# Performance work log

Measured on AMD Instinct MI355X. Metric: run time of the kernel, lower is better.

Reference implementation:

```python
import jax, jax.numpy as jnp
import numpy as np

GRID_SIZE = 100
N_GREEN = 524288
N_RED = 524288
LATENT_DIM = 10
HIDDEN = 128
IN_DIM = LATENT_DIM + 3 + 1  # z + level_data + loop index
TEMPERATURE = 500.0


def setup_inputs() -> dict:
    key = jax.random.key(0)
    ks = jax.random.split(key, 13)
    def lin(k, out_d, in_d):
        kw, kb = jax.random.split(k)
        s = 1.0 / np.sqrt(in_d)
        W = jax.random.uniform(kw, (out_d, in_d), jnp.float32, -s, s)
        b = jax.random.uniform(kb, (out_d,), jnp.float32, -s, s)
        return W, b
    z = jax.random.normal(ks[0], (LATENT_DIM,), jnp.float32)
    level_data = jnp.array([GRID_SIZE, N_GREEN, N_RED], dtype=jnp.int64)
    gW1, gb1 = lin(ks[1], HIDDEN, IN_DIM)
    gW2, gb2 = lin(ks[2], HIDDEN, HIDDEN)
    gW3, gb3 = lin(ks[3], 1, HIDDEN)
    rW1, rb1 = lin(ks[4], HIDDEN, IN_DIM)
    rW2, rb2 = lin(ks[5], HIDDEN, HIDDEN)
    rW3, rb3 = lin(ks[6], 1, HIDDEN)
    return {
        'z': z, 'level_data': level_data,
        'gW1': gW1, 'gb1': gb1, 'gW2': gW2, 'gb2': gb2, 'gW3': gW3, 'gb3': gb3,
        'rW1': rW1, 'rb1': rb1, 'rW2': rW2, 'rb2': rb2, 'rW3': rW3, 'rb3': rb3,
    }


def _mlp(x, W1, b1, W2, b2, W3, b3):
    # Linear -> LeakyReLU(0.2) -> Linear -> ELU(alpha=1) -> Linear
    h = jax.nn.leaky_relu(x @ W1.T + b1, negative_slope=0.2)
    h = jax.nn.elu(h @ W2.T + b2, alpha=1.0)
    return h @ W3.T + b3  # [N, 1]


def _coords(z_ext, n, W1, b1, W2, b2, W3, b3, scale):
    # batch all loop indices 0..n-1 into one GEMM call instead of n tiny launches
    idx = jnp.arange(n, dtype=jnp.float32)[:, None]            # [n, 1]
    x = jnp.concatenate(
        [jnp.broadcast_to(z_ext, (n, z_ext.shape[0])), idx], axis=1)  # [n, 14]
    out = _mlp(x, W1, b1, W2, b2, W3, b3)[:, 0]                 # [n]
    return (jax.nn.sigmoid(out / TEMPERATURE) * scale).astype(jnp.int32)


def reference(z, level_data, gW1, gb1, gW2, gb2, gW3, gb3,
              rW1, rb1, rW2, rb2, rW3, rb3):
    scale = level_data[0].astype(jnp.float32) ** 2 - 1.0  # grid_size^2 - 1
    z_ext = jnp.concatenate([z, level_data.astype(jnp.float32)])  # [13]
    coords_green = _coords(z_ext, N_GREEN, gW1, gb1, gW2, gb2, gW3, gb3, scale)
    coords_red = _coords(z_ext, N_RED, rW1, rb1, rW2, rb2, rW3, rb3, scale)
    return coords_green, coords_red
```

## Files before the change

kernel.cpp:

```cpp
#include <hip/hip_runtime.h>
#include <hip/hip_bf16.h>
#include <math.h>


#define HIDDEN 128
#define REGIONS 129
#define NEVT 512
#define CDSTRIDE (NEVT + 8)
#define CHUNK_SH 7
#define WS_HDR 16
#define TIMES_OFF   (WS_HDR)
#define TIMES(g,r)  (TIMES_OFF + ((g)*REGIONS + (r))*NEVT)
#define CTAB_OFF    (TIMES_OFF + 2*REGIONS*NEVT)
#define CTAB(g,r)   (CTAB_OFF + ((g)*REGIONS + (r))*CDSTRIDE)
#define DTAB_OFF    (CTAB_OFF + 2*REGIONS*CDSTRIDE)
#define DTAB(g,r)   (DTAB_OFF + ((g)*REGIONS + (r))*CDSTRIDE)
#define RTS_OFF     (DTAB_OFF + 2*REGIONS*CDSTRIDE)
#define RTS(g)      (RTS_OFF + (g)*REGIONS)
#define DIR_OFF     (RTS_OFF + 2*REGIONS + 16)

__device__ __constant__ float TH[4] = {-4.f, -1.8f, -0.7f, 0.f};
__device__ __constant__ float PM[5] = {0.f, 0.0668106f, 0.3011695f, 0.7191639f, 1.f};
__device__ __constant__ float PQ[5] = {-1.f, -0.7144420f, -0.2925961f, 0.f, 0.f};

__global__ __launch_bounds__(512) void build_kernel(
    const float* __restrict__ z, const int* __restrict__ level,
    const float* __restrict__ gW1, const float* __restrict__ gb1,
    const float* __restrict__ gW2, const float* __restrict__ gb2,
    const float* __restrict__ gW3, const float* __restrict__ gb3,
    const float* __restrict__ rW1, const float* __restrict__ rb1,
    const float* __restrict__ rW2, const float* __restrict__ rb2,
    const float* __restrict__ rW3, const float* __restrict__ rb3,
    float* __restrict__ ws, int* __restrict__ dir, int N, int nchunk)
{
    int g = blockIdx.x / REGIONS;
    int r = blockIdx.x - g * REGIONS;
    const float* W1 = g ? rW1 : gW1;  const float* b1 = g ? rb1 : gb1;
    const float* W2 = g ? rW2 : gW2;  const float* b2 = g ? rb2 : gb2;
    const float* W3 = g ? rW3 : gW3;  const float* b3 = g ? rb3 : gb3;

    __shared__ float zext[16];
    __shared__ float cs[HIDDEN], wv[HIDDEN], tb_l[HIDDEN], sts[HIDDEN];
    __shared__ float sc[HIDDEN], sw[HIDDEN], al[HIDDEN], be[HIDDEN];
    __shared__ float pa[4][HIDDEN], pb[4][HIDDEN];
    __shared__ float ev_t[NEVT], ev_c[NEVT], ev_d[NEVT];
    __shared__ float so_t[NEVT], pc_[NEVT], pd_[NEVT];
    __shared__ float c0s, d0s;
    __shared__ int cnt;
    int t = threadIdx.x;

    if (t == 0) {
        int g0 = level[0], l1 = level[1], l2 = level[2];
        if (l1 == 0) { l1 = level[2]; l2 = level[4]; }
        zext[10] = (float)g0; zext[11] = (float)l1; zext[12] = (float)l2;
        cnt = 0;
        if (blockIdx.x == 0) ws[0] = (float)g0 * (float)g0 - 1.0f;
    }
    if (t < 10) zext[t] = z[t];
    __syncthreads();

    if (t < HIDDEN) {
        float c = b1[t];
        #pragma unroll
        for (int q = 0; q < 13; ++q) c = fmaf(W1[t * 14 + q], zext[q], c);
        float w = W1[t * 14 + 13];
        cs[t] = c; wv[t] = w;
        float Nf = (float)N, tb = -c / w;
        if (!(tb > 0.0f)) tb = 0.0f;
        if (!(tb < Nf))  tb = Nf;
        tb_l[t] = tb;
    }
    __syncthreads();
    if (t < HIDDEN) {
        float tb = tb_l[t]; int rk = 0;
        for (int k = 0; k < HIDDEN; ++k) {
            float tk = tb_l[k];
            rk += (tk < tb || (tk == tb && k < t)) ? 1 : 0;
        }
        sts[rk] = tb;
    }
    __syncthreads();
    float i0 = (r == 0) ? 0.0f : sts[r - 1];
    float i1 = (r == REGIONS - 1) ? (float)N : sts[r];
    if (t == 0) ws[RTS(g) + r] = i1;

    if (t < HIDDEN) {
        float c = cs[t], w = wv[t];
        float mid = 0.5f * (i0 + i1);
        float s = (fmaf(mid, w, c) > 0.0f) ? 1.0f : 0.2f;
        sc[t] = s * c;  sw[t] = s * w;
    }
    __syncthreads();

    {
        int k = t & 127, q = t >> 7;
        float a = 0.0f, bb = 0.0f;
        const float4* row4 = (const float4*)(W2 + k * HIDDEN + q * 32);
        #pragma unroll
        for (int j4 = 0; j4 < 8; ++j4) {
            float4 w2 = row4[j4]; int j = q * 32 + j4 * 4;
            a = fmaf(w2.x, sc[j+0], a);  bb = fmaf(w2.x, sw[j+0], bb);
            a = fmaf(w2.y, sc[j+1], a);  bb = fmaf(w2.y, sw[j+1], bb);
            a = fmaf(w2.z, sc[j+2], a);  bb = fmaf(w2.z, sw[j+2], bb);
            a = fmaf(w2.w, sc[j+3], a);  bb = fmaf(w2.w, sw[j+3], bb);
        }
        pa[q][k] = a;  pb[q][k] = bb;
    }
    __syncthreads();
    if (t < HIDDEN) {
        al[t] = pa[0][t] + pa[1][t] + pa[2][t] + pa[3][t] + b2[t];
        be[t] = pb[0][t] + pb[1][t] + pb[2][t] + pb[3][t];
    }
    __syncthreads();

    {
        int ku = t >> 2, h = t & 3;
        float a = al[ku], b = be[ku], w3 = W3[ku];
        float p0 = fmaf(i0, b, a);
        int pcq = (p0 >= TH[0]) + (p0 >= TH[1]) + (p0 >= TH[2]) + (p0 >= TH[3]);
        bool up = (b > 0.0f), dn = (b < 0.0f);
        bool dir_ok = up ? (h >= pcq) : (dn && (h < pcq));
        float tc = (TH[h] - a) / b;
        if (dir_ok && (tc <= i1)) {
            float dm, dq;
            if (up) { dm = PM[h+1] - PM[h]; dq = PQ[h+1] - PQ[h]; }
            else    { dm = PM[h] - PM[h+1]; dq = PQ[h] - PQ[h+1]; }
            int pos = atomicAdd(&cnt, 1);
            ev_t[pos] = tc;
            ev_c[pos] = w3 * fmaf(dm, a, dq);
            ev_d[pos] = w3 * dm * b;
        }
    }
    if (t < HIDDEN) {
        float a = al[t], b = be[t], w3 = W3[t];
        float p0 = fmaf(i0, b, a);
        int pp = (p0 >= TH[0]) + (p0 >= TH[1]) + (p0 >= TH[2]) + (p0 >= TH[3]);
        pa[0][t] = w3 * fmaf(PM[pp], a, PQ[pp]);
        pb[0][t] = w3 * PM[pp] * b;
    }
    __syncthreads();
    int m = cnt;

    if (t < 64) {
        float sA = pa[0][t] + pa[0][t + 64];
        float sB = pb[0][t] + pb[0][t + 64];
        #pragma unroll
        for (int off = 32; off >= 1; off >>= 1) {
            sA += __shfl_down(sA, off);
            sB += __shfl_down(sB, off);
        }
        if (t == 0) { c0s = sA + b3[0]; d0s = sB; }
    }
    if (t < m) {
        float myt = ev_t[t]; int rk = 0;
        for (int e = 0; e < m; ++e) {
            float te = ev_t[e];
            rk += (te < myt || (te == myt && e < t)) ? 1 : 0;
        }
        so_t[rk] = myt;  pc_[rk] = ev_c[t];  pd_[rk] = ev_d[t];
    }
    __syncthreads();
    if (t == 0) {
        float vc = 0.0f, vd = 0.0f;
        for (int e = 0; e < m; ++e) { vc += pc_[e]; vd += pd_[e]; pc_[e] = vc; pd_[e] = vd; }
    }
    __syncthreads();

    float C0 = c0s, D0 = d0s;
    float totc = (m > 0) ? pc_[m - 1] : 0.0f;
    float totd = (m > 0) ? pd_[m - 1] : 0.0f;
    float* Tt = ws + TIMES(g, r);
    float* Tc = ws + CTAB(g, r);
    float* Td = ws + DTAB(g, r);
    Tt[t]     = (t < m) ? so_t[t] : INFINITY;
    Tc[t + 1] = C0 + ((t < m) ? pc_[t] : totc);
    Td[t + 1] = D0 + ((t < m) ? pd_[t] : totd);
    if (t == 0) { Tc[0] = C0; Td[0] = D0; }

    int qlo = ((int)i0) >> CHUNK_SH;
    for (int q = qlo + t; ; q += 512) {
        float fc = (float)(q << CHUNK_SH);
        if (!(fc < i1)) break;
        if (fc >= i0 && q < nchunk) {
            int a = 0;
            for (int e = 0; e < m; ++e) a += (so_t[e] <= fc) ? 1 : 0;
            dir[g * nchunk + q] = (r << 16) | a;
        }
    }
}

__global__ __launch_bounds__(256) void gen_kernel(
    const float* __restrict__ ws, const int* __restrict__ dir,
    int* __restrict__ out, int N, int total, int nchunk)
{
    int e0 = (blockIdx.x * 256 + threadIdx.x) * 4;
    if (e0 >= total) return;
    int g = (e0 >= N) ? 1 : 0;
    int i = e0 - g * N;

    int pd = dir[g * nchunk + (i >> CHUNK_SH)];
    int r = pd >> 16, a = pd & 0xffff;
    const float* Tt = ws + TIMES(g, r);
    const float* Tc = ws + CTAB(g, r);
    const float* Td = ws + DTAB(g, r);
    const float* RT = ws + RTS(g);
    float rtEnd = RT[r];
    float nextT = Tt[a];
    float C = Tc[a], D = Td[a];
    float scale = ws[0];

    int4 res;
    #pragma unroll
    for (int q = 0; q < 4; ++q) {
        float fi = (float)(i + q);
        while (fi >= rtEnd) {
            ++r; a = 0;
            Tt = ws + TIMES(g, r); Tc = ws + CTAB(g, r); Td = ws + DTAB(g, r);
            rtEnd = RT[r]; nextT = Tt[0]; C = Tc[0]; D = Td[0];
        }
        while (nextT <= fi) {
            ++a; nextT = Tt[a]; C = Tc[a]; D = Td[a];
        }
        float o = fmaf(fi, D, C);
        float sg = 1.0f / (1.0f + __expf(-o * (1.0f / 500.0f)));
        ((int*)&res)[q] = (int)(sg * scale);
    }
    ((int4*)out)[e0 >> 2] = res;
}

extern "C" void kernel_launch(void* const* d_in, const int* in_sizes, int n_in,
                              void* d_out, int out_size, void* d_ws, size_t ws_size,
                              hipStream_t stream) {
    const float* z   = (const float*)d_in[0];
    const int* level = (const int*)d_in[1];
    const float* gW1 = (const float*)d_in[2];
    const float* gb1 = (const float*)d_in[3];
    const float* gW2 = (const float*)d_in[4];
    const float* gb2 = (const float*)d_in[5];
    const float* gW3 = (const float*)d_in[6];
    const float* gb3 = (const float*)d_in[7];
    const float* rW1 = (const float*)d_in[8];
    const float* rb1 = (const float*)d_in[9];
    const float* rW2 = (const float*)d_in[10];
    const float* rb2 = (const float*)d_in[11];
    const float* rW3 = (const float*)d_in[12];
    const float* rb3 = (const float*)d_in[13];
    int* out  = (int*)d_out;
    float* ws = (float*)d_ws;
    int* dir  = (int*)(ws + DIR_OFF);
    int N = out_size / 2;
    int nchunk = (N + (1 << CHUNK_SH) - 1) >> CHUNK_SH;

    build_kernel<<<2 * REGIONS, 512, 0, stream>>>(z, level,
        gW1, gb1, gW2, gb2, gW3, gb3, rW1, rb1, rW2, rb2, rW3, rb3,
        ws, dir, N, nchunk);
    gen_kernel<<<(out_size / 4 + 255) / 256, 256, 0, stream>>>(ws, dir, out,
                                                               N, out_size, nchunk);
}
```

Measured before the change: 94.44 us.

## Fuse build and generate kernels into per-slice piecewise-linear evaluation

Replaces the two-kernel scheme (global region build, then table-driven generation) with one kernel. Each block covers a 1024-element slice and finds the layer-1 breakpoints inside it. For each resulting segment it recomputes the layer-2 affine coefficients and the event list, then evaluates its outputs directly from shared memory. This removes the second launch and the workspace round-trip. In exchange every block of the roughly 1024 launched redoes the W1/W2 matvecs and the event sort per segment, so total compute is much higher.

```diff
diff --git a/kernel.cpp b/kernel.cpp
--- a/kernel.cpp
+++ b/kernel.cpp
@@ -1,29 +1,17 @@
 #include <hip/hip_runtime.h>
-#include <hip/hip_bf16.h>
 #include <math.h>
 
 
 #define HIDDEN 128
-#define REGIONS 129
-#define NEVT 512
-#define CDSTRIDE (NEVT + 8)
-#define CHUNK_SH 7
-#define WS_HDR 16
-#define TIMES_OFF   (WS_HDR)
-#define TIMES(g,r)  (TIMES_OFF + ((g)*REGIONS + (r))*NEVT)
-#define CTAB_OFF    (TIMES_OFF + 2*REGIONS*NEVT)
-#define CTAB(g,r)   (CTAB_OFF + ((g)*REGIONS + (r))*CDSTRIDE)
-#define DTAB_OFF    (CTAB_OFF + 2*REGIONS*CDSTRIDE)
-#define DTAB(g,r)   (DTAB_OFF + ((g)*REGIONS + (r))*CDSTRIDE)
-#define RTS_OFF     (DTAB_OFF + 2*REGIONS*CDSTRIDE)
-#define RTS(g)      (RTS_OFF + (g)*REGIONS)
-#define DIR_OFF     (RTS_OFF + 2*REGIONS + 16)
+#define BLK 256
+#define SLICE 1024
+#define MAXEV 512
 
 __device__ __constant__ float TH[4] = {-4.f, -1.8f, -0.7f, 0.f};
 __device__ __constant__ float PM[5] = {0.f, 0.0668106f, 0.3011695f, 0.7191639f, 1.f};
 __device__ __constant__ float PQ[5] = {-1.f, -0.7144420f, -0.2925961f, 0.f, 0.f};
 
-__global__ __launch_bounds__(512) void build_kernel(
+__global__ __launch_bounds__(BLK) void fused_kernel(
     const float* __restrict__ z, const int* __restrict__ level,
     const float* __restrict__ gW1, const float* __restrict__ gb1,
     const float* __restrict__ gW2, const float* __restrict__ gb2,
@@ -31,30 +19,36 @@
     const float* __restrict__ rW1, const float* __restrict__ rb1,
     const float* __restrict__ rW2, const float* __restrict__ rb2,
     const float* __restrict__ rW3, const float* __restrict__ rb3,
-    float* __restrict__ ws, int* __restrict__ dir, int N, int nchunk)
+    int* __restrict__ out, int N, int total)
 {
-    int g = blockIdx.x / REGIONS;
-    int r = blockIdx.x - g * REGIONS;
+    __shared__ float zext[16];
+    __shared__ float cs[HIDDEN], wv[HIDDEN];
+    __shared__ float sc[HIDDEN], sw[HIDDEN], al[HIDDEN], be[HIDDEN];
+    __shared__ float pA[2][HIDDEN], pB[2][HIDDEN];
+    __shared__ float sA[HIDDEN], sB[HIDDEN];
+    __shared__ float bps[HIDDEN], bss[HIDDEN];
+    __shared__ float ev_t[MAXEV], ev_c[MAXEV], ev_d[MAXEV];
+    __shared__ float so_t[MAXEV], pc_[MAXEV], pd_[MAXEV];
+    __shared__ float c0s, d0s;
+    __shared__ int cnt, bcnt;
+
+    int t = threadIdx.x;
+    int gbase = blockIdx.x * SLICE;
+    int g = (gbase >= N) ? 1 : 0;
+    int s0 = gbase - g * N;
+    int s1 = s0 + SLICE; if (s1 > N) s1 = N;
+    float s0f = (float)s0, s1f = (float)s1;
+
     const float* W1 = g ? rW1 : gW1;  const float* b1 = g ? rb1 : gb1;
     const float* W2 = g ? rW2 : gW2;  const float* b2 = g ? rb2 : gb2;
     const float* W3 = g ? rW3 : gW3;  const float* b3 = g ? rb3 : gb3;
-
-    __shared__ float zext[16];
-    __shared__ float cs[HIDDEN], wv[HIDDEN], tb_l[HIDDEN], sts[HIDDEN];
-    __shared__ float sc[HIDDEN], sw[HIDDEN], al[HIDDEN], be[HIDDEN];
-    __shared__ float pa[4][HIDDEN], pb[4][HIDDEN];
-    __shared__ float ev_t[NEVT], ev_c[NEVT], ev_d[NEVT];
-    __shared__ float so_t[NEVT], pc_[NEVT], pd_[NEVT];
-    __shared__ float c0s, d0s;
-    __shared__ int cnt;
-    int t = threadIdx.x;
 
     if (t == 0) {
         int g0 = level[0], l1 = level[1], l2 = level[2];
         if (l1 == 0) { l1 = level[2]; l2 = level[4]; }
         zext[10] = (float)g0; zext[11] = (float)l1; zext[12] = (float)l2;
-        cnt = 0;
-        if (blockIdx.x == 0) ws[0] = (float)g0 * (float)g0 - 1.0f;
+        zext[13] = (float)g0 * (float)g0 - 1.0f;
+        bcnt = 0;
     }
     if (t < 10) zext[t] = z[t];
     __syncthreads();
@@ -65,167 +59,133 @@
         for (int q = 0; q < 13; ++q) c = fmaf(W1[t * 14 + q], zext[q], c);
         float w = W1[t * 14 + 13];
         cs[t] = c; wv[t] = w;
-        float Nf = (float)N, tb = -c / w;
-        if (!(tb > 0.0f)) tb = 0.0f;
-        if (!(tb < Nf))  tb = Nf;
-        tb_l[t] = tb;
+        float tb = -c / w;
+        if (tb > s0f && tb < s1f) {
+            int p = atomicAdd(&bcnt, 1);
+            bps[p] = tb;
+        }
     }
     __syncthreads();
-    if (t < HIDDEN) {
-        float tb = tb_l[t]; int rk = 0;
-        for (int k = 0; k < HIDDEN; ++k) {
-            float tk = tb_l[k];
-            rk += (tk < tb || (tk == tb && k < t)) ? 1 : 0;
-        }
-        sts[rk] = tb;
+    int nb = bcnt;
+    if (t < nb) {
+        float myt = bps[t]; int rk = 0;
+        for (int e = 0; e < nb; ++e) {
+            float te = bps[e];
+            rk += (te < myt || (te == myt && e < t)) ? 1 : 0;
+        }
+        bss[rk] = myt;
     }
     __syncthreads();
-    float i0 = (r == 0) ? 0.0f : sts[r - 1];
-    float i1 = (r == REGIONS - 1) ? (float)N : sts[r];
-    if (t == 0) ws[RTS(g) + r] = i1;
-
-    if (t < HIDDEN) {
-        float c = cs[t], w = wv[t];
-        float mid = 0.5f * (i0 + i1);
-        float s = (fmaf(mid, w, c) > 0.0f) ? 1.0f : 0.2f;
-        sc[t] = s * c;  sw[t] = s * w;
-    }
-    __syncthreads();
-
-    {
-        int k = t & 127, q = t >> 7;
-        float a = 0.0f, bb = 0.0f;
-        const float4* row4 = (const float4*)(W2 + k * HIDDEN + q * 32);
+
+    float scale = zext[13];
+    int4 res = make_int4(0, 0, 0, 0);
+    int ibase = s0 + t * 4;
+
+    for (int seg = 0; seg <= nb; ++seg) {
+        float i0 = (seg == 0) ? s0f : bss[seg - 1];
+        float i1 = (seg == nb) ? s1f : bss[seg];
+
+        if (t < HIDDEN) {
+            float mid = 0.5f * (i0 + i1);
+            float s = (fmaf(mid, wv[t], cs[t]) > 0.0f) ? 1.0f : 0.2f;
+            sc[t] = s * cs[t];  sw[t] = s * wv[t];
+        }
+        if (t == 0) cnt = 0;
+        __syncthreads();
+
+        {
+            int k = t & 127, qq = t >> 7;
+            float a = 0.0f, bb = 0.0f;
+            const float4* row4 = (const float4*)(W2 + k * HIDDEN + qq * 64);
+            #pragma unroll
+            for (int j4 = 0; j4 < 16; ++j4) {
+                float4 w2 = row4[j4]; int j = qq * 64 + j4 * 4;
+                a = fmaf(w2.x, sc[j+0], a);  bb = fmaf(w2.x, sw[j+0], bb);
+                a = fmaf(w2.y, sc[j+1], a);  bb = fmaf(w2.y, sw[j+1], bb);
+                a = fmaf(w2.z, sc[j+2], a);  bb = fmaf(w2.z, sw[j+2], bb);
+                a = fmaf(w2.w, sc[j+3], a);  bb = fmaf(w2.w, sw[j+3], bb);
+            }
+            pA[qq][k] = a;  pB[qq][k] = bb;
+        }
+        __syncthreads();
+        if (t < HIDDEN) {
+            al[t] = pA[0][t] + pA[1][t] + b2[t];
+            be[t] = pB[0][t] + pB[1][t];
+        }
+        __syncthreads();
+
+        for (int e = t; e < 512; e += BLK) {
+            int ku = e >> 2, h = e & 3;
+            float a = al[ku], b = be[ku], w3 = W3[ku];
+            float p0 = fmaf(i0, b, a);
+            int pcq = (p0 >= TH[0]) + (p0 >= TH[1]) + (p0 >= TH[2]) + (p0 >= TH[3]);
+            bool up = (b > 0.0f), dn = (b < 0.0f);
+            bool ok = up ? (h >= pcq) : (dn && (h < pcq));
+            float tc = (TH[h] - a) / b;
+            if (ok && tc <= i1) {
+                float dm, dq;
+                if (up) { dm = PM[h+1] - PM[h]; dq = PQ[h+1] - PQ[h]; }
+                else    { dm = PM[h] - PM[h+1]; dq = PQ[h] - PQ[h+1]; }
+                int pos = atomicAdd(&cnt, 1);
+                ev_t[pos] = tc;
+                ev_c[pos] = w3 * fmaf(dm, a, dq);
+                ev_d[pos] = w3 * dm * b;
+            }
+        }
+        if (t < HIDDEN) {
+            float a = al[t], b = be[t], w3 = W3[t];
+            float p0 = fmaf(i0, b, a);
+            int pp = (p0 >= TH[0]) + (p0 >= TH[1]) + (p0 >= TH[2]) + (p0 >= TH[3]);
+            sA[t] = w3 * fmaf(PM[pp], a, PQ[pp]);
+            sB[t] = w3 * PM[pp] * b;
+        }
+        __syncthreads();
+        int m = cnt;
+
+        if (t < 64) {
+            float rA = sA[t] + sA[t + 64];
+            float rB = sB[t] + sB[t + 64];
+            #pragma unroll
+            for (int off = 32; off >= 1; off >>= 1) {
+                rA += __shfl_down(rA, off);
+                rB += __shfl_down(rB, off);
+            }
+            if (t == 0) { c0s = rA + b3[0]; d0s = rB; }
+        }
+        for (int ei = t; ei < m; ei += BLK) {
+            float myt = ev_t[ei]; int rk = 0;
+            for (int e = 0; e < m; ++e) {
+                float te = ev_t[e];
+                rk += (te < myt || (te == myt && e < ei)) ? 1 : 0;
+            }
+            so_t[rk] = myt;  pc_[rk] = ev_c[ei];  pd_[rk] = ev_d[ei];
+        }
+        __syncthreads();
+        if (t == 0) {
+            float vc = 0.0f, vd = 0.0f;
+            for (int e = 0; e < m; ++e) { vc += pc_[e]; vd += pd_[e]; pc_[e] = vc; pd_[e] = vd; }
+        }
+        __syncthreads();
+
+        float C0 = c0s, D0 = d0s;
         #pragma unroll
-        for (int j4 = 0; j4 < 8; ++j4) {
-            float4 w2 = row4[j4]; int j = q * 32 + j4 * 4;
-            a = fmaf(w2.x, sc[j+0], a);  bb = fmaf(w2.x, sw[j+0], bb);
-            a = fmaf(w2.y, sc[j+1], a);  bb = fmaf(w2.y, sw[j+1], bb);
-            a = fmaf(w2.z, sc[j+2], a);  bb = fmaf(w2.z, sw[j+2], bb);
-            a = fmaf(w2.w, sc[j+3], a);  bb = fmaf(w2.w, sw[j+3], bb);
-        }
-        pa[q][k] = a;  pb[q][k] = bb;
-    }
-    __syncthreads();
-    if (t < HIDDEN) {
-        al[t] = pa[0][t] + pa[1][t] + pa[2][t] + pa[3][t] + b2[t];
-        be[t] = pb[0][t] + pb[1][t] + pb[2][t] + pb[3][t];
-    }
-    __syncthreads();
-
-    {
-        int ku = t >> 2, h = t & 3;
-        float a = al[ku], b = be[ku], w3 = W3[ku];
-        float p0 = fmaf(i0, b, a);
-        int pcq = (p0 >= TH[0]) + (p0 >= TH[1]) + (p0 >= TH[2]) + (p0 >= TH[3]);
-        bool up = (b > 0.0f), dn = (b < 0.0f);
-        bool dir_ok = up ? (h >= pcq) : (dn && (h < pcq));
-        float tc = (TH[h] - a) / b;
-        if (dir_ok && (tc <= i1)) {
-            float dm, dq;
-            if (up) { dm = PM[h+1] - PM[h]; dq = PQ[h+1] - PQ[h]; }
-            else    { dm = PM[h] - PM[h+1]; dq = PQ[h] - PQ[h+1]; }
-            int pos = atomicAdd(&cnt, 1);
-            ev_t[pos] = tc;
-            ev_c[pos] = w3 * fmaf(dm, a, dq);
-            ev_d[pos] = w3 * dm * b;
-        }
-    }
-    if (t < HIDDEN) {
-        float a = al[t], b = be[t], w3 = W3[t];
-        float p0 = fmaf(i0, b, a);
-        int pp = (p0 >= TH[0]) + (p0 >= TH[1]) + (p0 >= TH[2]) + (p0 >= TH[3]);
-        pa[0][t] = w3 * fmaf(PM[pp], a, PQ[pp]);
-        pb[0][t] = w3 * PM[pp] * b;
-    }
-    __syncthreads();
-    int m = cnt;
-
-    if (t < 64) {
-        float sA = pa[0][t] + pa[0][t + 64];
-        float sB = pb[0][t] + pb[0][t + 64];
-        #pragma unroll
-        for (int off = 32; off >= 1; off >>= 1) {
-            sA += __shfl_down(sA, off);
-            sB += __shfl_down(sB, off);
-        }
-        if (t == 0) { c0s = sA + b3[0]; d0s = sB; }
-    }
-    if (t < m) {
-        float myt = ev_t[t]; int rk = 0;
-        for (int e = 0; e < m; ++e) {
-            float te = ev_t[e];
-            rk += (te < myt || (te == myt && e < t)) ? 1 : 0;
-        }
-        so_t[rk] = myt;  pc_[rk] = ev_c[t];  pd_[rk] = ev_d[t];
-    }
-    __syncthreads();
-    if (t == 0) {
-        float vc = 0.0f, vd = 0.0f;
-        for (int e = 0; e < m; ++e) { vc += pc_[e]; vd += pd_[e]; pc_[e] = vc; pd_[e] = vd; }
-    }
-    __syncthreads();
-
-    float C0 = c0s, D0 = d0s;
-    float totc = (m > 0) ? pc_[m - 1] : 0.0f;
-    float totd = (m > 0) ? pd_[m - 1] : 0.0f;
-    float* Tt = ws + TIMES(g, r);
-    float* Tc = ws + CTAB(g, r);
-    float* Td = ws + DTAB(g, r);
-    Tt[t]     = (t < m) ? so_t[t] : INFINITY;
-    Tc[t + 1] = C0 + ((t < m) ? pc_[t] : totc);
-    Td[t + 1] = D0 + ((t < m) ? pd_[t] : totd);
-    if (t == 0) { Tc[0] = C0; Td[0] = D0; }
-
-    int qlo = ((int)i0) >> CHUNK_SH;
-    for (int q = qlo + t; ; q += 512) {
-        float fc = (float)(q << CHUNK_SH);
-        if (!(fc < i1)) break;
-        if (fc >= i0 && q < nchunk) {
-            int a = 0;
-            for (int e = 0; e < m; ++e) a += (so_t[e] <= fc) ? 1 : 0;
-            dir[g * nchunk + q] = (r << 16) | a;
-        }
-    }
-}
-
-__global__ __launch_bounds__(256) void gen_kernel(
-    const float* __restrict__ ws, const int* __restrict__ dir,
-    int* __restrict__ out, int N, int total, int nchunk)
-{
-    int e0 = (blockIdx.x * 256 + threadIdx.x) * 4;
-    if (e0 >= total) return;
-    int g = (e0 >= N) ? 1 : 0;
-    int i = e0 - g * N;
-
-    int pd = dir[g * nchunk + (i >> CHUNK_SH)];
-    int r = pd >> 16, a = pd & 0xffff;
-    const float* Tt = ws + TIMES(g, r);
-    const float* Tc = ws + CTAB(g, r);
-    const float* Td = ws + DTAB(g, r);
-    const float* RT = ws + RTS(g);
-    float rtEnd = RT[r];
-    float nextT = Tt[a];
-    float C = Tc[a], D = Td[a];
-    float scale = ws[0];
-
-    int4 res;
-    #pragma unroll
-    for (int q = 0; q < 4; ++q) {
-        float fi = (float)(i + q);
-        while (fi >= rtEnd) {
-            ++r; a = 0;
-            Tt = ws + TIMES(g, r); Tc = ws + CTAB(g, r); Td = ws + DTAB(g, r);
-            rtEnd = RT[r]; nextT = Tt[0]; C = Tc[0]; D = Td[0];
-        }
-        while (nextT <= fi) {
-            ++a; nextT = Tt[a]; C = Tc[a]; D = Td[a];
-        }
-        float o = fmaf(fi, D, C);
-        float sg = 1.0f / (1.0f + __expf(-o * (1.0f / 500.0f)));
-        ((int*)&res)[q] = (int)(sg * scale);
-    }
-    ((int4*)out)[e0 >> 2] = res;
+        for (int q = 0; q < 4; ++q) {
+            float fi = (float)(ibase + q);
+            if (fi >= i0 && fi < i1) {
+                float C = C0, D = D0;
+                for (int e = 0; e < m; ++e) {
+                    if (so_t[e] <= fi) { C = C0 + pc_[e]; D = D0 + pd_[e]; }
+                }
+                float o = fmaf(fi, D, C);
+                float sg = 1.0f / (1.0f + __expf(-o * (1.0f / 500.0f)));
+                ((int*)&res)[q] = (int)(sg * scale);
+            }
+        }
+        __syncthreads();
+    }
+
+    int oidx = gbase + t * 4;
+    if (oidx < total) ((int4*)out)[oidx >> 2] = res;
 }
 
 extern "C" void kernel_launch(void* const* d_in, const int* in_sizes, int n_in,
@@ -245,15 +205,12 @@
     const float* rb2 = (const float*)d_in[11];
     const float* rW3 = (const float*)d_in[12];
     const float* rb3 = (const float*)d_in[13];
-    int* out  = (int*)d_out;
-    float* ws = (float*)d_ws;
-    int* dir  = (int*)(ws + DIR_OFF);
+    int* out = (int*)d_out;
     int N = out_size / 2;
-    int nchunk = (N + (1 << CHUNK_SH) - 1) >> CHUNK_SH;
-
-    build_kernel<<<2 * REGIONS, 512, 0, stream>>>(z, level,
+    int total = out_size;
+    int nblocks = (total + SLICE - 1) / SLICE;
+
+    fused_kernel<<<nblocks, BLK, 0, stream>>>(z, level,
         gW1, gb1, gW2, gb2, gW3, gb3, rW1, rb1, rW2, rb2, rW3, rb3,
-        ws, dir, N, nchunk);
-    gen_kernel<<<(out_size / 4 + 255) / 256, 256, 0, stream>>>(ws, dir, out,
-                                                               N, out_size, nchunk);
+        out, N, total);
 }
```

New measurement: 94.31 us. About the same (-0.1%).
